# Kernel optimization log

Hardware: AMD Instinct MI355X
Metric: run time of the kernel (lower is better)

The kernel has to match this reference:

```python
import jax, jax.numpy as jnp
import numpy as np

B, M, N = 128, 512, 512
THRESH = 0.5  # parsed from stop_strategy 'threshold_0.5'
AVG_DEG = 16.0


def setup_inputs() -> dict:
    key = jax.random.key(0)
    k1, k2, k3 = jax.random.split(key, 3)
    y_pred = jax.random.uniform(k1, (B, M, N), dtype=jnp.float32)

    def make_adj(k, n):
        a = (jax.random.uniform(k, (B, n, n)) < (AVG_DEG / n)).astype(jnp.float32)
        a = jnp.maximum(a, jnp.swapaxes(a, 1, 2))          # symmetric
        return a * (1.0 - jnp.eye(n, dtype=jnp.float32))   # no self loops

    return {"y_pred": y_pred, "adj1": make_adj(k2, M), "adj2": make_adj(k3, N)}


def _frontier(adj, v):
    # neighbors of selected nodes that are not yet selected
    return jnp.minimum(adj @ v, 1.0) * (1.0 - v)


def _search_one(y, a1, a2):
    """Greedy MCS tree search for one graph pair. y: (M,N), a1: (M,M), a2: (N,N)."""
    m, n = y.shape

    def cond(s):
        return s[0]

    def body(s):
        cont, v1, v2, tree, fmask = s
        masked = y * fmask
        mx = jnp.max(masked)
        new_cont = mx >= THRESH                 # stop check BEFORE commit (original order)
        idx = jnp.argmax(masked)
        i, j = idx // n, idx % n
        v1n = v1.at[i].set(1.0)
        v2n = v2.at[j].set(1.0)
        treen = tree.at[i, j].set(1.0)
        fmn = _frontier(a1, v1n)[:, None] * _frontier(a2, v2n)[None, :]
        pick = lambda new, old: jnp.where(new_cont, new, old)
        return (new_cont, pick(v1n, v1), pick(v2n, v2), pick(treen, tree), pick(fmn, fmask))

    init = (jnp.array(True),
            jnp.zeros((m,), jnp.float32),
            jnp.zeros((n,), jnp.float32),
            jnp.zeros((m, n), jnp.float32),
            jnp.ones((m, n), jnp.float32))
    final = jax.lax.while_loop(cond, body, init)
    return final[3]  # tree_pred match matrix


@jax.jit
def _search_batch(y_pred, adj1, adj2):
    return jax.vmap(_search_one)(y_pred, adj1, adj2)


def reference(y_pred, adj1, adj2):
    # returns the tree_pred match matrices for every pair in the batch
    return _search_batch(y_pred, adj1, adj2)
```

## Files before the change

### kernel.cpp

```cpp
#include <hip/hip_runtime.h>
#include <stdint.h>

#define MDIM 512
#define NDIM 512
#define NTHREADS 512

typedef unsigned long long u64;

__device__ __forceinline__ u64 wave_max_u64(u64 v) {
#pragma unroll
  for (int off = 32; off; off >>= 1) {
    u64 q = __shfl_xor(v, off);
    if (q > v) v = q;
  }
  return v;
}

__global__ __launch_bounds__(256) void transpose_kernel(
    const float* __restrict__ in, float* __restrict__ out)
{
  __shared__ float tile[32][33];
  const int b = blockIdx.z;
  const float* __restrict__ I = in  + (size_t)b * (MDIM * NDIM);
  float* __restrict__ O       = out + (size_t)b * (MDIM * NDIM);
  const int x  = blockIdx.x * 32 + threadIdx.x;
  const int y0 = blockIdx.y * 32 + threadIdx.y;
#pragma unroll
  for (int dy = 0; dy < 32; dy += 8)
    tile[threadIdx.y + dy][threadIdx.x] = I[(size_t)(y0 + dy) * NDIM + x];
  __syncthreads();
  const int xo = blockIdx.y * 32 + threadIdx.x;
  const int yo = blockIdx.x * 32 + threadIdx.y;
#pragma unroll
  for (int dy = 0; dy < 32; dy += 8)
    O[(size_t)(yo + dy) * MDIM + xo] = tile[threadIdx.x][threadIdx.y + dy];
}

__global__ __launch_bounds__(NTHREADS, 1) void tree_search_kernel(
    const float* __restrict__ y,
    const float* __restrict__ yt,
    const float* __restrict__ a1,
    const float* __restrict__ a2,
    float* __restrict__ out)
{
  const int b   = blockIdx.x;
  const int tid = threadIdx.x;
  const float* __restrict__ Y  = y  + (size_t)b * (MDIM * NDIM);
  const float* __restrict__ YT = yt ? yt + (size_t)b * (MDIM * NDIM) : nullptr;
  const float* __restrict__ A1 = a1 + (size_t)b * (MDIM * MDIM);
  const float* __restrict__ A2 = a2 + (size_t)b * (NDIM * NDIM);
  float* __restrict__ O = out + (size_t)b * (MDIM * NDIM);

  __shared__ unsigned rowState[MDIM];
  __shared__ float    rowMax[MDIM];
  __shared__ unsigned rowArg[MDIM];
  __shared__ unsigned colState[NDIM];
  __shared__ unsigned colList[NDIM];
  __shared__ unsigned colPos[NDIM];
  __shared__ unsigned newCols[NDIM];
  __shared__ unsigned addRows[MDIM];
  __shared__ int s_colCount, s_nAdd, s_nNew, s_stop, s_ci, s_cj;
  __shared__ u64 s_part[NTHREADS / 64];

  rowState[tid] = 0u;
  colState[tid] = 0u;
  rowMax[tid]   = 0.f;
  rowArg[tid]   = 511u;
  if (tid == 0) { s_colCount = 0; s_nAdd = 0; s_nNew = 0; s_stop = 0; }
  __syncthreads();

  {
    u64 best = 0;
    for (int base = tid * 4; base < MDIM * NDIM; base += NTHREADS * 4) {
      const float4 v = *reinterpret_cast<const float4*>(Y + base);
      const float vv[4] = {v.x, v.y, v.z, v.w};
#pragma unroll
      for (int c = 0; c < 4; ++c) {
        u64 p = ((u64)__float_as_uint(vv[c]) << 32)
                | (u64)(262143u - (unsigned)(base + c));
        if (p > best) best = p;
      }
    }
    best = wave_max_u64(best);
    if ((tid & 63) == 0) s_part[tid >> 6] = best;
    __syncthreads();
    if (tid == 0) {
      u64 bst = s_part[0];
#pragma unroll
      for (int w = 1; w < NTHREADS / 64; ++w) if (s_part[w] > bst) bst = s_part[w];
      float v = __uint_as_float((unsigned)(bst >> 32));
      if (v >= 0.5f) {
        unsigned key = 262143u - (unsigned)(bst & 0xFFFFFFFFu);
        int bi = key >> 9, bj = key & 511;
        rowState[bi] = 3u;
        colState[bj] = 2u;
        O[key] = 1.0f;
        s_ci = bi; s_cj = bj;
      } else {
        s_stop = 1;
      }
    }
    __syncthreads();
  }

  while (!s_stop) {
    {
      const int r = tid;
      const unsigned st = rowState[r];
      const float av = A1[(size_t)s_ci * MDIM + r];
      const bool newRow   = (av != 0.f) && (st == 0u);
      const bool recompute = (st == 1u) && (rowArg[r] == (unsigned)s_cj);
      if (newRow || recompute) {
        rowState[r] = 2u;
        addRows[atomicAdd(&s_nAdd, 1)] = (unsigned)r;
      }
      const float bv = A2[(size_t)s_cj * NDIM + r];
      if (bv != 0.f && colState[r] == 0u) {
        colState[r] = 1u;
        newCols[atomicAdd(&s_nNew, 1)] = (unsigned)r;
        int p = atomicAdd(&s_colCount, 1);
        colList[p] = (unsigned)r;
        colPos[r]  = (unsigned)p;
      }
    }
    __syncthreads();

    {
      const int r = tid;
      const bool active = (rowState[r] == 1u);
      float rm = rowMax[r];
      unsigned ra = rowArg[r];
      const int nn = s_nNew;
      if (YT) {
        for (int k = 0; k < nn; ++k) {
          const unsigned c = newCols[k];
          const float v = YT[((unsigned)c << 9) + (unsigned)r];
          if (active && (v > rm || (v == rm && c < ra))) { rm = v; ra = c; }
        }
      } else {
        for (int k = 0; k < nn; ++k) {
          const unsigned c = newCols[k];
          const float v = Y[((unsigned)r << 9) + c];
          if (active && (v > rm || (v == rm && c < ra))) { rm = v; ra = c; }
        }
      }
      if (active) { rowMax[r] = rm; rowArg[r] = ra; }
    }
    __syncthreads();

    {
      const int g = tid >> 3, lane = tid & 7;
      const int nAdd = s_nAdd, cc = s_colCount;
      for (int a = g; a < nAdd; a += NTHREADS / 8) {
        const int rr = (int)addRows[a];
        float rm = 0.f;
        unsigned ra = 511u;
        for (int k = lane; k < cc; k += 8) {
          const unsigned c = colList[k];
          const float v = Y[((unsigned)rr << 9) + c];
          if (v > rm || (v == rm && c < ra)) { rm = v; ra = c; }
        }
        u64 p = ((u64)__float_as_uint(rm) << 32) | (u64)(511u - ra);
#pragma unroll
        for (int off = 4; off; off >>= 1) {
          u64 q = __shfl_xor(p, off, 8);
          if (q > p) p = q;
        }
        if (lane == 0) {
          rowMax[rr]   = __uint_as_float((unsigned)(p >> 32));
          rowArg[rr]   = 511u - (unsigned)(p & 0xFFFFFFFFu);
          rowState[rr] = 1u;
        }
      }
    }
    __syncthreads();

    {
      u64 cand = 0;
      if (rowState[tid] == 1u) {
        const unsigned key = ((unsigned)tid << 9) | rowArg[tid];
        cand = ((u64)__float_as_uint(rowMax[tid]) << 32)
               | (u64)(262143u - key);
      }
      cand = wave_max_u64(cand);
      if ((tid & 63) == 0) s_part[tid >> 6] = cand;
    }
    __syncthreads();

    if (tid == 0) {
      u64 bst = s_part[0];
#pragma unroll
      for (int w = 1; w < NTHREADS / 64; ++w) if (s_part[w] > bst) bst = s_part[w];
      const float v = __uint_as_float((unsigned)(bst >> 32));
      if (v >= 0.5f) {
        const unsigned key = 262143u - (unsigned)(bst & 0xFFFFFFFFu);
        const int bi = key >> 9, bj = key & 511;
        rowState[bi] = 3u;
        colState[bj] = 2u;
        const int p    = (int)colPos[bj];
        const int last = (int)colList[s_colCount - 1];
        colList[p]    = (unsigned)last;
        colPos[last]  = (unsigned)p;
        s_colCount--;
        O[key] = 1.0f;
        s_ci = bi; s_cj = bj;
        s_nAdd = 0; s_nNew = 0;
      } else {
        s_stop = 1;
      }
    }
    __syncthreads();
  }
}

extern "C" void kernel_launch(void* const* d_in, const int* in_sizes, int n_in,
                              void* d_out, int out_size, void* d_ws, size_t ws_size,
                              hipStream_t stream) {
  const float* y  = (const float*)d_in[0];
  const float* a1 = (const float*)d_in[1];
  const float* a2 = (const float*)d_in[2];
  float* out = (float*)d_out;
  const int B = in_sizes[0] / (MDIM * NDIM);

  (void)hipMemsetAsync(d_out, 0, (size_t)out_size * sizeof(float), stream);

  const size_t yt_bytes = (size_t)B * MDIM * NDIM * sizeof(float);
  float* yt = nullptr;
  if (ws_size >= yt_bytes) {
    yt = (float*)d_ws;
    dim3 tb(32, 8, 1), tg(NDIM / 32, MDIM / 32, B);
    transpose_kernel<<<tg, tb, 0, stream>>>(y, yt);
  }
  tree_search_kernel<<<B, NTHREADS, 0, stream>>>(y, yt, a1, a2, out);
}
```

Before: 3.701 ms.

## Rewrite tree search as single-wave kernel with adjacency bitmasks and per-row top-k

The 512-thread search block is replaced by a single 64-lane wave per batch item, so the per-iteration block barriers and shared atomics go away. Adjacency matrices are precomputed into bitmasks in shared memory by a separate kernel. A top-k kernel stores each row's 32 largest scores, so newly added rows can usually take their best free column from that list instead of rescanning. Small launches run at low occupancy, and one wave does the per-row work serially.

```diff
diff --git a/kernel.cpp b/kernel.cpp
--- a/kernel.cpp
+++ b/kernel.cpp
@@ -1,13 +1,13 @@
 #include <hip/hip_runtime.h>
 #include <stdint.h>
 
-#define MDIM 512
-#define NDIM 512
-#define NTHREADS 512
+#define MD 512
+#define B_ELEMS (MD * MD)
+#define TOPK 32
 
 typedef unsigned long long u64;
 
-__device__ __forceinline__ u64 wave_max_u64(u64 v) {
+__device__ __forceinline__ u64 bfly64_max(u64 v) {
 #pragma unroll
   for (int off = 32; off; off >>= 1) {
     u64 q = __shfl_xor(v, off);
@@ -21,195 +21,330 @@
 {
   __shared__ float tile[32][33];
   const int b = blockIdx.z;
-  const float* __restrict__ I = in  + (size_t)b * (MDIM * NDIM);
-  float* __restrict__ O       = out + (size_t)b * (MDIM * NDIM);
+  const float* __restrict__ I = in  + (size_t)b * B_ELEMS;
+  float* __restrict__ O       = out + (size_t)b * B_ELEMS;
   const int x  = blockIdx.x * 32 + threadIdx.x;
   const int y0 = blockIdx.y * 32 + threadIdx.y;
 #pragma unroll
   for (int dy = 0; dy < 32; dy += 8)
-    tile[threadIdx.y + dy][threadIdx.x] = I[(size_t)(y0 + dy) * NDIM + x];
+    tile[threadIdx.y + dy][threadIdx.x] = I[(size_t)(y0 + dy) * MD + x];
   __syncthreads();
   const int xo = blockIdx.y * 32 + threadIdx.x;
   const int yo = blockIdx.x * 32 + threadIdx.y;
 #pragma unroll
   for (int dy = 0; dy < 32; dy += 8)
-    O[(size_t)(yo + dy) * MDIM + xo] = tile[threadIdx.x][threadIdx.y + dy];
-}
-
-__global__ __launch_bounds__(NTHREADS, 1) void tree_search_kernel(
+    O[(size_t)(yo + dy) * MD + xo] = tile[threadIdx.x][threadIdx.y + dy];
+}
+
+__global__ __launch_bounds__(256) void bits_kernel(
+    const float* __restrict__ a1, const float* __restrict__ a2,
+    u64* __restrict__ b1, u64* __restrict__ b2)
+{
+  const int wave = threadIdx.x >> 6, lane = threadIdx.x & 63;
+  const int r = blockIdx.x * 4 + wave;
+  const int b = blockIdx.y;
+  const size_t rowoff = ((size_t)b * MD + r) * MD;
+#pragma unroll
+  for (int k = 0; k < 8; ++k) {
+    const u64 m1 = __ballot(a1[rowoff + (k << 6) + lane] != 0.f);
+    const u64 m2 = __ballot(a2[rowoff + (k << 6) + lane] != 0.f);
+    if (lane == 0) {
+      b1[((size_t)b * MD + r) * 8 + k] = m1;
+      b2[((size_t)b * MD + r) * 8 + k] = m2;
+    }
+  }
+}
+
+__global__ __launch_bounds__(256) void topk_kernel(
+    const float* __restrict__ y, u64* __restrict__ top)
+{
+  const int wave = threadIdx.x >> 6, lane = threadIdx.x & 63;
+  const size_t row = (size_t)blockIdx.x * 4 + wave;
+  const float* __restrict__ Yr = y + row * MD;
+  const int c0 = lane * 8;
+  const float4 va = *reinterpret_cast<const float4*>(Yr + c0);
+  const float4 vb = *reinterpret_cast<const float4*>(Yr + c0 + 4);
+  const float vv[8] = {va.x, va.y, va.z, va.w, vb.x, vb.y, vb.z, vb.w};
+  u64 p[8];
+#pragma unroll
+  for (int j = 0; j < 8; ++j)
+    p[j] = ((u64)__float_as_uint(vv[j]) << 32) | (u64)(511 - (c0 + j));
+  u64* __restrict__ dst = top + row * TOPK;
+  for (int t = 0; t < TOPK; ++t) {
+    u64 lb = p[0];
+#pragma unroll
+    for (int j = 1; j < 8; ++j) if (p[j] > lb) lb = p[j];
+    const u64 g = bfly64_max(lb);
+    if (lb == g && g != 0) {
+#pragma unroll
+      for (int j = 0; j < 8; ++j) if (p[j] == g) p[j] = 0;
+      dst[t] = g;
+    } else if (lane == 0 && g == 0) {
+      dst[t] = 0;
+    }
+  }
+}
+
+__global__ __launch_bounds__(64, 1) void search_kernel(
     const float* __restrict__ y,
     const float* __restrict__ yt,
+    const u64*  __restrict__ gb1,
+    const u64*  __restrict__ gb2,
+    const u64*  __restrict__ gtop,
     const float* __restrict__ a1,
     const float* __restrict__ a2,
     float* __restrict__ out)
 {
-  const int b   = blockIdx.x;
-  const int tid = threadIdx.x;
-  const float* __restrict__ Y  = y  + (size_t)b * (MDIM * NDIM);
-  const float* __restrict__ YT = yt ? yt + (size_t)b * (MDIM * NDIM) : nullptr;
-  const float* __restrict__ A1 = a1 + (size_t)b * (MDIM * MDIM);
-  const float* __restrict__ A2 = a2 + (size_t)b * (NDIM * NDIM);
-  float* __restrict__ O = out + (size_t)b * (MDIM * NDIM);
-
-  __shared__ unsigned rowState[MDIM];
-  __shared__ float    rowMax[MDIM];
-  __shared__ unsigned rowArg[MDIM];
-  __shared__ unsigned colState[NDIM];
-  __shared__ unsigned colList[NDIM];
-  __shared__ unsigned colPos[NDIM];
-  __shared__ unsigned newCols[NDIM];
-  __shared__ unsigned addRows[MDIM];
-  __shared__ int s_colCount, s_nAdd, s_nNew, s_stop, s_ci, s_cj;
-  __shared__ u64 s_part[NTHREADS / 64];
-
-  rowState[tid] = 0u;
-  colState[tid] = 0u;
-  rowMax[tid]   = 0.f;
-  rowArg[tid]   = 511u;
-  if (tid == 0) { s_colCount = 0; s_nAdd = 0; s_nNew = 0; s_stop = 0; }
-  __syncthreads();
-
-  {
-    u64 best = 0;
-    for (int base = tid * 4; base < MDIM * NDIM; base += NTHREADS * 4) {
-      const float4 v = *reinterpret_cast<const float4*>(Y + base);
-      const float vv[4] = {v.x, v.y, v.z, v.w};
-#pragma unroll
-      for (int c = 0; c < 4; ++c) {
-        u64 p = ((u64)__float_as_uint(vv[c]) << 32)
-                | (u64)(262143u - (unsigned)(base + c));
-        if (p > best) best = p;
-      }
-    }
-    best = wave_max_u64(best);
-    if ((tid & 63) == 0) s_part[tid >> 6] = best;
-    __syncthreads();
-    if (tid == 0) {
-      u64 bst = s_part[0];
-#pragma unroll
-      for (int w = 1; w < NTHREADS / 64; ++w) if (s_part[w] > bst) bst = s_part[w];
-      float v = __uint_as_float((unsigned)(bst >> 32));
-      if (v >= 0.5f) {
-        unsigned key = 262143u - (unsigned)(bst & 0xFFFFFFFFu);
-        int bi = key >> 9, bj = key & 511;
-        rowState[bi] = 3u;
-        colState[bj] = 2u;
-        O[key] = 1.0f;
-        s_ci = bi; s_cj = bj;
-      } else {
-        s_stop = 1;
-      }
-    }
-    __syncthreads();
-  }
-
-  while (!s_stop) {
-    {
-      const int r = tid;
+  const int b = blockIdx.x;
+  const int lane = threadIdx.x;
+  const float* __restrict__ Y  = y + (size_t)b * B_ELEMS;
+  const float* __restrict__ YT = yt ? yt + (size_t)b * B_ELEMS : nullptr;
+  const u64*  __restrict__ TP  = gtop ? gtop + (size_t)b * MD * TOPK : nullptr;
+  float* __restrict__ O = out + (size_t)b * B_ELEMS;
+
+  __shared__ u64 lb1[MD * 8];
+  __shared__ u64 lb2[MD * 8];
+  __shared__ u64 rowPack[MD];
+  __shared__ unsigned rowState[MD];
+  __shared__ unsigned colState[MD];
+  __shared__ unsigned colList[MD];
+  __shared__ unsigned colPos[MD];
+  __shared__ unsigned pendList[MD];
+
+  if (gb1) {
+    const u64* s1 = gb1 + (size_t)b * MD * 8;
+    const u64* s2 = gb2 + (size_t)b * MD * 8;
+    for (int i = lane; i < MD * 8; i += 64) { lb1[i] = s1[i]; lb2[i] = s2[i]; }
+  } else {
+    const float* A1 = a1 + (size_t)b * B_ELEMS;
+    const float* A2 = a2 + (size_t)b * B_ELEMS;
+    for (int r = 0; r < MD; ++r) {
+#pragma unroll
+      for (int k = 0; k < 8; ++k) {
+        const u64 m1 = __ballot(A1[(size_t)r * MD + (k << 6) + lane] != 0.f);
+        const u64 m2 = __ballot(A2[(size_t)r * MD + (k << 6) + lane] != 0.f);
+        if (lane == 0) { lb1[(r << 3) + k] = m1; lb2[(r << 3) + k] = m2; }
+      }
+    }
+  }
+  for (int i = lane; i < MD; i += 64) {
+    rowState[i] = 0u; colState[i] = 0u; rowPack[i] = 0ull;
+  }
+
+  u64 best0 = 0;
+  if (TP) {
+#pragma unroll
+    for (int k = 0; k < 8; ++k) {
+      const int r = (k << 6) + lane;
+      const u64 e = TP[(size_t)r * TOPK];
+      const unsigned c = 511u - (unsigned)(e & 0x1FFu);
+      const u64 cand = (e & 0xFFFFFFFF00000000ull)
+                     | (u64)(262143u - (((unsigned)r << 9) | c));
+      if (cand > best0) best0 = cand;
+    }
+  } else {
+    for (int base = lane * 16; base < B_ELEMS; base += 64 * 16) {
+#pragma unroll
+      for (int q = 0; q < 4; ++q) {
+        const float4 v = *reinterpret_cast<const float4*>(Y + base + q * 4);
+        const float vv[4] = {v.x, v.y, v.z, v.w};
+#pragma unroll
+        for (int j = 0; j < 4; ++j) {
+          const u64 pkd = ((u64)__float_as_uint(vv[j]) << 32)
+                        | (u64)(262143u - (unsigned)(base + q * 4 + j));
+          if (pkd > best0) best0 = pkd;
+        }
+      }
+    }
+  }
+  best0 = bfly64_max(best0);
+  if (__uint_as_float((unsigned)(best0 >> 32)) < 0.5f) return;
+  const unsigned key0 = 262143u - (unsigned)(best0 & 0xFFFFFFFFu);
+  int ci = key0 >> 9, cj = key0 & 511;
+  if (lane == 0) { rowState[ci] = 3u; colState[cj] = 2u; O[key0] = 1.0f; }
+  int colCount = 0;
+
+  while (true) {
+    const int prevCount = colCount;
+    int nPend = 0;
+#pragma unroll
+    for (int k = 0; k < 8; ++k) {
+      const int r = (k << 6) + lane;
+      const bool adj = (lb1[(ci << 3) + k] >> lane) & 1ull;
       const unsigned st = rowState[r];
-      const float av = A1[(size_t)s_ci * MDIM + r];
-      const bool newRow   = (av != 0.f) && (st == 0u);
-      const bool recompute = (st == 1u) && (rowArg[r] == (unsigned)s_cj);
-      if (newRow || recompute) {
-        rowState[r] = 2u;
-        addRows[atomicAdd(&s_nAdd, 1)] = (unsigned)r;
-      }
-      const float bv = A2[(size_t)s_cj * NDIM + r];
-      if (bv != 0.f && colState[r] == 0u) {
-        colState[r] = 1u;
-        newCols[atomicAdd(&s_nNew, 1)] = (unsigned)r;
-        int p = atomicAdd(&s_colCount, 1);
-        colList[p] = (unsigned)r;
-        colPos[r]  = (unsigned)p;
-      }
-    }
-    __syncthreads();
-
-    {
-      const int r = tid;
-      const bool active = (rowState[r] == 1u);
-      float rm = rowMax[r];
-      unsigned ra = rowArg[r];
-      const int nn = s_nNew;
-      if (YT) {
-        for (int k = 0; k < nn; ++k) {
-          const unsigned c = newCols[k];
-          const float v = YT[((unsigned)c << 9) + (unsigned)r];
-          if (active && (v > rm || (v == rm && c < ra))) { rm = v; ra = c; }
+      bool mk = false;
+      if (st == 1u) {
+        const unsigned argc = 511u - (unsigned)(rowPack[r] & 0x1FFu);
+        mk = (argc == (unsigned)cj);
+      } else if (st == 0u) {
+        mk = adj;
+      }
+      if (mk) rowState[r] = 2u;
+      const u64 mP = __ballot(mk);
+      if (lane == 0) {
+        u64 m = mP; int idx = nPend;
+        while (m) { const int l = __builtin_ctzll(m); m &= m - 1;
+                    pendList[idx++] = (unsigned)((k << 6) + l); }
+      }
+      nPend += (int)__popcll(mP);
+    }
+#pragma unroll
+    for (int k = 0; k < 8; ++k) {
+      const int c = (k << 6) + lane;
+      const bool cadj = (lb2[(cj << 3) + k] >> lane) & 1ull;
+      const bool isnew = cadj && (colState[c] == 0u);
+      if (isnew) colState[c] = 1u;
+      const u64 mN = __ballot(isnew);
+      if (lane == 0) {
+        u64 m = mN; int idx = colCount;
+        while (m) { const int l = __builtin_ctzll(m); m &= m - 1;
+                    const int cc2 = (k << 6) + l;
+                    colList[idx] = (unsigned)cc2; colPos[cc2] = (unsigned)idx; ++idx; }
+      }
+      colCount += (int)__popcll(mN);
+    }
+
+    const int nNew = colCount - prevCount;
+    if (nNew > 0) {
+      unsigned st8[8]; u64 pk8[8];
+      bool anyLocal = false;
+#pragma unroll
+      for (int k = 0; k < 8; ++k) {
+        const int r = (k << 6) + lane;
+        st8[k] = rowState[r];
+        pk8[k] = rowPack[r];
+        anyLocal |= (st8[k] == 1u);
+      }
+      if (__ballot(anyLocal) != 0ull) {
+        for (int i = 0; i < nNew; i += 4) {
+          const int c0 = (int)colList[prevCount + i];
+          const int c1 = (i + 1 < nNew) ? (int)colList[prevCount + i + 1] : c0;
+          const int c2 = (i + 2 < nNew) ? (int)colList[prevCount + i + 2] : c0;
+          const int c3 = (i + 3 < nNew) ? (int)colList[prevCount + i + 3] : c0;
+          float v0[8], v1[8], v2[8], v3[8];
+          if (YT) {
+#pragma unroll
+            for (int k = 0; k < 8; ++k) {
+              const int r = (k << 6) + lane;
+              v0[k] = YT[(size_t)c0 * MD + r];
+              v1[k] = YT[(size_t)c1 * MD + r];
+              v2[k] = YT[(size_t)c2 * MD + r];
+              v3[k] = YT[(size_t)c3 * MD + r];
+            }
+          } else {
+#pragma unroll
+            for (int k = 0; k < 8; ++k) {
+              const int r = (k << 6) + lane;
+              v0[k] = Y[(size_t)r * MD + c0];
+              v1[k] = Y[(size_t)r * MD + c1];
+              v2[k] = Y[(size_t)r * MD + c2];
+              v3[k] = Y[(size_t)r * MD + c3];
+            }
+          }
+#pragma unroll
+          for (int k = 0; k < 8; ++k) {
+            if (st8[k] == 1u) {
+              u64 cp = ((u64)__float_as_uint(v0[k]) << 32) | (u64)(511 - c0);
+              if (cp > pk8[k]) pk8[k] = cp;
+              if (i + 1 < nNew) {
+                cp = ((u64)__float_as_uint(v1[k]) << 32) | (u64)(511 - c1);
+                if (cp > pk8[k]) pk8[k] = cp;
+              }
+              if (i + 2 < nNew) {
+                cp = ((u64)__float_as_uint(v2[k]) << 32) | (u64)(511 - c2);
+                if (cp > pk8[k]) pk8[k] = cp;
+              }
+              if (i + 3 < nNew) {
+                cp = ((u64)__float_as_uint(v3[k]) << 32) | (u64)(511 - c3);
+                if (cp > pk8[k]) pk8[k] = cp;
+              }
+            }
+          }
+        }
+#pragma unroll
+        for (int k = 0; k < 8; ++k)
+          if (st8[k] == 1u) rowPack[(k << 6) + lane] = pk8[k];
+      }
+    }
+
+    if (nPend > 0) {
+      if (nPend >= 5) {
+        const int g = lane >> 3, l8 = lane & 7;
+        for (int a = g; a < nPend; a += 8) {
+          const int rr = (int)pendList[a];
+          const float* Yr = Y + (size_t)rr * MD;
+          u64 bb = 0;
+          for (int k2 = l8; k2 < colCount; k2 += 8) {
+            const int c = (int)colList[k2];
+            const u64 cp = ((u64)__float_as_uint(Yr[c]) << 32) | (u64)(511 - c);
+            if (cp > bb) bb = cp;
+          }
+#pragma unroll
+          for (int off = 4; off; off >>= 1) {
+            const u64 q = __shfl_xor(bb, off, 8);
+            if (q > bb) bb = q;
+          }
+          if (l8 == 0) { rowPack[rr] = bb; rowState[rr] = 1u; }
         }
       } else {
-        for (int k = 0; k < nn; ++k) {
-          const unsigned c = newCols[k];
-          const float v = Y[((unsigned)r << 9) + c];
-          if (active && (v > rm || (v == rm && c < ra))) { rm = v; ra = c; }
+        for (int a = 0; a < nPend; ++a) {
+          const int rr = (int)pendList[a];
+          bool done = false;
+          if (TP) {
+            u64 e = 0; bool valid = false;
+            if (lane < TOPK) {
+              e = TP[(size_t)rr * TOPK + lane];
+              const int c = 511 - (int)(e & 0x1FFu);
+              valid = (colState[c] == 1u);
+            }
+            const u64 mb = __ballot(valid);
+            if (mb) {
+              const int first = __builtin_ctzll(mb);
+              const u64 win = __shfl(e, first);
+              if (lane == 0) { rowPack[rr] = win; rowState[rr] = 1u; }
+              done = true;
+            }
+          }
+          if (!done) {
+            const float* Yr = Y + (size_t)rr * MD;
+            u64 bb = 0;
+            for (int k2 = lane; k2 < colCount; k2 += 64) {
+              const int c = (int)colList[k2];
+              const u64 cp = ((u64)__float_as_uint(Yr[c]) << 32) | (u64)(511 - c);
+              if (cp > bb) bb = cp;
+            }
+            bb = bfly64_max(bb);
+            if (lane == 0) { rowPack[rr] = bb; rowState[rr] = 1u; }
+          }
         }
       }
-      if (active) { rowMax[r] = rm; rowArg[r] = ra; }
-    }
-    __syncthreads();
-
-    {
-      const int g = tid >> 3, lane = tid & 7;
-      const int nAdd = s_nAdd, cc = s_colCount;
-      for (int a = g; a < nAdd; a += NTHREADS / 8) {
-        const int rr = (int)addRows[a];
-        float rm = 0.f;
-        unsigned ra = 511u;
-        for (int k = lane; k < cc; k += 8) {
-          const unsigned c = colList[k];
-          const float v = Y[((unsigned)rr << 9) + c];
-          if (v > rm || (v == rm && c < ra)) { rm = v; ra = c; }
-        }
-        u64 p = ((u64)__float_as_uint(rm) << 32) | (u64)(511u - ra);
-#pragma unroll
-        for (int off = 4; off; off >>= 1) {
-          u64 q = __shfl_xor(p, off, 8);
-          if (q > p) p = q;
-        }
-        if (lane == 0) {
-          rowMax[rr]   = __uint_as_float((unsigned)(p >> 32));
-          rowArg[rr]   = 511u - (unsigned)(p & 0xFFFFFFFFu);
-          rowState[rr] = 1u;
-        }
-      }
-    }
-    __syncthreads();
-
-    {
-      u64 cand = 0;
-      if (rowState[tid] == 1u) {
-        const unsigned key = ((unsigned)tid << 9) | rowArg[tid];
-        cand = ((u64)__float_as_uint(rowMax[tid]) << 32)
-               | (u64)(262143u - key);
-      }
-      cand = wave_max_u64(cand);
-      if ((tid & 63) == 0) s_part[tid >> 6] = cand;
-    }
-    __syncthreads();
-
-    if (tid == 0) {
-      u64 bst = s_part[0];
-#pragma unroll
-      for (int w = 1; w < NTHREADS / 64; ++w) if (s_part[w] > bst) bst = s_part[w];
-      const float v = __uint_as_float((unsigned)(bst >> 32));
-      if (v >= 0.5f) {
-        const unsigned key = 262143u - (unsigned)(bst & 0xFFFFFFFFu);
-        const int bi = key >> 9, bj = key & 511;
-        rowState[bi] = 3u;
-        colState[bj] = 2u;
-        const int p    = (int)colPos[bj];
-        const int last = (int)colList[s_colCount - 1];
-        colList[p]    = (unsigned)last;
-        colPos[last]  = (unsigned)p;
-        s_colCount--;
-        O[key] = 1.0f;
-        s_ci = bi; s_cj = bj;
-        s_nAdd = 0; s_nNew = 0;
-      } else {
-        s_stop = 1;
-      }
-    }
-    __syncthreads();
+    }
+
+    u64 bc = 0;
+#pragma unroll
+    for (int k = 0; k < 8; ++k) {
+      const int r = (k << 6) + lane;
+      if (rowState[r] == 1u) {
+        const u64 pk = rowPack[r];
+        const unsigned arg = 511u - (unsigned)(pk & 0x1FFu);
+        const u64 cand = (pk & 0xFFFFFFFF00000000ull)
+                       | (u64)(262143u - (((unsigned)r << 9) | arg));
+        if (cand > bc) bc = cand;
+      }
+    }
+    bc = bfly64_max(bc);
+    if (__uint_as_float((unsigned)(bc >> 32)) < 0.5f) break;
+    const unsigned key = 262143u - (unsigned)(bc & 0xFFFFFFFFu);
+    const int bi = key >> 9, bj = key & 511;
+    if (lane == 0) {
+      rowState[bi] = 3u; colState[bj] = 2u;
+      const int p = (int)colPos[bj];
+      const unsigned last = colList[colCount - 1];
+      colList[p] = last; colPos[last] = (unsigned)p;
+      O[key] = 1.0f;
+    }
+    --colCount;
+    ci = bi; cj = bj;
   }
 }
 
@@ -220,16 +355,27 @@
   const float* a1 = (const float*)d_in[1];
   const float* a2 = (const float*)d_in[2];
   float* out = (float*)d_out;
-  const int B = in_sizes[0] / (MDIM * NDIM);
+  const int B = in_sizes[0] / B_ELEMS;
 
   (void)hipMemsetAsync(d_out, 0, (size_t)out_size * sizeof(float), stream);
 
-  const size_t yt_bytes = (size_t)B * MDIM * NDIM * sizeof(float);
-  float* yt = nullptr;
-  if (ws_size >= yt_bytes) {
-    yt = (float*)d_ws;
-    dim3 tb(32, 8, 1), tg(NDIM / 32, MDIM / 32, B);
+  char* wsp = (char*)d_ws;
+  size_t off = 0;
+  const size_t ytB  = (size_t)B * B_ELEMS * sizeof(float);
+  const size_t topB = (size_t)B * MD * TOPK * sizeof(u64);
+  const size_t bitB = (size_t)B * MD * 8 * sizeof(u64);
+  float* yt = nullptr; u64* top = nullptr; u64* b1 = nullptr; u64* b2 = nullptr;
+  if (ws_size >= off + ytB)      { yt  = (float*)(wsp + off); off += ytB;  }
+  if (ws_size >= off + topB)     { top = (u64*)  (wsp + off); off += topB; }
+  if (ws_size >= off + 2 * bitB) { b1  = (u64*)  (wsp + off); off += bitB;
+                                   b2  = (u64*)  (wsp + off); off += bitB; }
+
+  if (yt) {
+    dim3 tb(32, 8, 1), tg(MD / 32, MD / 32, B);
     transpose_kernel<<<tg, tb, 0, stream>>>(y, yt);
   }
-  tree_search_kernel<<<B, NTHREADS, 0, stream>>>(y, yt, a1, a2, out);
-}
+  if (b1) bits_kernel<<<dim3(MD / 4, B), 256, 0, stream>>>(a1, a2, b1, b2);
+  if (top) topk_kernel<<<dim3(B * (MD / 4)), 256, 0, stream>>>(y, top);
+
+  search_kernel<<<B, 64, 0, stream>>>(y, yt, b1, b2, top, a1, a2, out);
+}
```

Measured after the change: 3.266 ms. 11.8% less time.
